# Performance work log

Hardware: AMD Instinct MI355X
Metric: run time of the kernel (lower is better)

The kernel has to match this reference:

```python
import jax, jax.numpy as jnp
import numpy as np

D_MODEL = 1024
NUM_HEADS = 16
D_K = D_MODEL // NUM_HEADS


def setup_inputs() -> dict:
    key = jax.random.key(0)
    ks = jax.random.split(key, 5)
    B, S = 4, 2048
    scale = 1.0 / np.sqrt(D_MODEL)
    x = jax.random.normal(ks[0], (B, S, D_MODEL), dtype=jnp.float32)
    Wq = jax.random.normal(ks[1], (D_MODEL, D_MODEL), dtype=jnp.float32) * scale
    Wk = jax.random.normal(ks[2], (D_MODEL, D_MODEL), dtype=jnp.float32) * scale
    Wv = jax.random.normal(ks[3], (D_MODEL, D_MODEL), dtype=jnp.float32) * scale
    Wo = jax.random.normal(ks[4], (D_MODEL, D_MODEL), dtype=jnp.float32) * scale
    return {"x": x, "Wq": Wq, "Wk": Wk, "Wv": Wv, "Wo": Wo}


def reference(x, Wq, Wk, Wv, Wo):
    B, S, _ = x.shape
    # projections (torch Linear: y = x @ W^T, no bias)
    def proj(W):
        y = jnp.einsum('bsd,ed->bse', x, W)
        # split heads: (b, s, h*dk) -> (b, h, s, dk)
        return y.reshape(B, S, NUM_HEADS, D_K).transpose(0, 2, 1, 3)
    Q, K, V = proj(Wq), proj(Wk), proj(Wv)
    scores = jnp.einsum('bhqd,bhkd->bhqk', Q, K) / np.sqrt(D_K)
    causal = jnp.tril(jnp.ones((S, S), dtype=bool))
    scores = jnp.where(causal, scores, -jnp.inf)
    attn = jax.nn.softmax(scores, axis=-1)
    out = jnp.einsum('bhqk,bhkd->bhqd', attn, V)
    out = out.transpose(0, 2, 1, 3).reshape(B, S, D_MODEL)
    return jnp.einsum('bse,de->bsd', out, Wo)
```

## Files before the change

### kernel.cpp

```cpp
#include <hip/hip_runtime.h>
#include <hip/hip_bf16.h>

typedef __attribute__((ext_vector_type(8))) short short8;
typedef __attribute__((ext_vector_type(4))) float f32x4;
typedef __attribute__((ext_vector_type(16))) float f32x16;

static constexpr int DM = 1024;
static constexpr int NH = 16;
static constexpr int DK = 64;
static constexpr int SL = 2048;
static constexpr int BB = 4;
static constexpr size_t QKV_ELEMS = (size_t)BB * NH * SL * DK;
static constexpr float NEG_BIG = -30000.0f;
static constexpr float SC_LOG2E = 0.125f * 1.44269504088896340736f;

union PackB { __hip_bfloat16 h[8]; uint4 u; };
union Pack4 { __hip_bfloat16 h[4]; uint2 u; };

typedef __attribute__((address_space(1))) unsigned int gu32;
typedef __attribute__((address_space(3))) unsigned int lu32;
__device__ __forceinline__ void async_copy16(const void* g, void* l) {
    __builtin_amdgcn_global_load_lds((gu32*)g, (lu32*)l, 16, 0, 0);
}

__device__ __forceinline__ unsigned cvt_pk_bf16(float lo, float hi) {
    unsigned r;
    asm("v_cvt_pk_bf16_f32 %0, %1, %2" : "=v"(r) : "v"(lo), "v"(hi));
    return r;
}
__device__ __forceinline__ void pl32_swap(unsigned &a, unsigned &b) {
    asm("v_permlane32_swap_b32 %0, %1" : "+v"(a), "+v"(b));
}

__global__ __launch_bounds__(256)
void cvt_all(const float* __restrict__ x,
             const float* __restrict__ wq, const float* __restrict__ wk,
             const float* __restrict__ wv, const float* __restrict__ wo,
             __hip_bfloat16* __restrict__ dst)
{
    const size_t i = (size_t)blockIdx.x * 256 + threadIdx.x;
    const float* src; size_t local;
    if (i < 2097152) { src = x; local = i; }
    else {
        const size_t j = i - 2097152;
        const int r = (int)(j >> 18);
        local = j & 262143;
        src = (r == 0) ? wq : (r == 1) ? wk : (r == 2) ? wv : wo;
    }
    float4 f = reinterpret_cast<const float4*>(src)[local];
    Pack4 p;
    p.h[0] = __float2bfloat16(f.x); p.h[1] = __float2bfloat16(f.y);
    p.h[2] = __float2bfloat16(f.z); p.h[3] = __float2bfloat16(f.w);
    reinterpret_cast<uint2*>(dst)[i] = p.u;
}

__global__ __launch_bounds__(256)
void gemm_qkv(const __hip_bfloat16* __restrict__ A,
              const __hip_bfloat16* __restrict__ W,
              __hip_bfloat16* __restrict__ q_out,
              __hip_bfloat16* __restrict__ k_out,
              __hip_bfloat16* __restrict__ v_out)
{
    __shared__ __hip_bfloat16 As[128 * 64];
    __shared__ __hip_bfloat16 Bs[128 * 64];
    const int tid  = threadIdx.x;
    const int m0   = blockIdx.x * 128;
    const int n0   = blockIdx.y * 128;
    const int w    = tid >> 6;
    const int lane = tid & 63;
    const int quad = lane >> 4;
    const int ln   = lane & 15;
    const int wm   = (w & 1) * 64;
    const int wn   = (w >> 1) * 64;
    const int srow = lane >> 3;
    const int sch  = ((lane & 7) ^ srow) * 8;

    f32x4 acc[4][4] = {};

    for (int k0 = 0; k0 < DM; k0 += 64) {
        #pragma unroll
        for (int j = 0; j < 4; j++) {
            const int rbase = w * 32 + j * 8;
            async_copy16(A + (size_t)(m0 + rbase + srow) * DM + k0 + sch,
                         &As[rbase * 64]);
            async_copy16(W + (size_t)(n0 + rbase + srow) * DM + k0 + sch,
                         &Bs[rbase * 64]);
        }
        __syncthreads();

        #pragma unroll
        for (int ks = 0; ks < 2; ks++) {
            short8 a[4], b[4];
            #pragma unroll
            for (int i = 0; i < 4; i++)
                a[i] = *reinterpret_cast<const short8*>(
                    &As[(wm + i*16 + ln) * 64 + (((ks*4 + quad) ^ (ln & 7)) * 8)]);
            #pragma unroll
            for (int j = 0; j < 4; j++)
                b[j] = *reinterpret_cast<const short8*>(
                    &Bs[(wn + j*16 + ln) * 64 + (((ks*4 + quad) ^ (ln & 7)) * 8)]);
            #pragma unroll
            for (int i = 0; i < 4; i++)
                #pragma unroll
                for (int j = 0; j < 4; j++)
                    acc[i][j] = __builtin_amdgcn_mfma_f32_16x16x32_bf16(a[i], b[j], acc[i][j], 0, 0, 0);
        }
        __syncthreads();
    }

    #pragma unroll
    for (int i = 0; i < 4; i++) {
        #pragma unroll
        for (int j = 0; j < 4; j++) {
            #pragma unroll
            for (int r = 0; r < 4; r++) {
                const int m = m0 + wm + i*16 + quad*4 + r;
                const int n = n0 + wn + j*16 + ln;
                const int b_ = m >> 11;
                const int s  = m & 2047;
                const int which = n >> 10;
                const int nn = n & 1023;
                const int h  = nn >> 6;
                const int d  = nn & 63;
                const __hip_bfloat16 v = __float2bfloat16(acc[i][j][r]);
                if (which == 0)
                    q_out[((size_t)((b_*NH + h)*SL + s))*DK + d] = v;
                else if (which == 1)
                    k_out[((size_t)((b_*NH + h)*SL + s))*DK + d] = v;
                else
                    v_out[((size_t)((b_*NH + h)*DK + d))*SL + s] = v;
            }
        }
    }
}

__global__ __launch_bounds__(256)
void gemm_wo(const __hip_bfloat16* __restrict__ A,
             const __hip_bfloat16* __restrict__ W,
             float* __restrict__ outp)
{
    __shared__ __hip_bfloat16 As[128 * 64];
    __shared__ __hip_bfloat16 Bs[128 * 64];
    const int tid  = threadIdx.x;
    const int m0   = blockIdx.x * 128;
    const int n0   = blockIdx.y * 128;
    const int w    = tid >> 6;
    const int lane = tid & 63;
    const int quad = lane >> 4;
    const int ln   = lane & 15;
    const int wm   = (w & 1) * 64;
    const int wn   = (w >> 1) * 64;
    const int srow = lane >> 3;
    const int sch  = ((lane & 7) ^ srow) * 8;

    f32x4 acc[4][4] = {};

    for (int k0 = 0; k0 < DM; k0 += 64) {
        #pragma unroll
        for (int j = 0; j < 4; j++) {
            const int rbase = w * 32 + j * 8;
            async_copy16(A + (size_t)(m0 + rbase + srow) * DM + k0 + sch,
                         &As[rbase * 64]);
            async_copy16(W + (size_t)(n0 + rbase + srow) * DM + k0 + sch,
                         &Bs[rbase * 64]);
        }
        __syncthreads();

        #pragma unroll
        for (int ks = 0; ks < 2; ks++) {
            short8 a[4], b[4];
            #pragma unroll
            for (int i = 0; i < 4; i++)
                a[i] = *reinterpret_cast<const short8*>(
                    &As[(wm + i*16 + ln) * 64 + (((ks*4 + quad) ^ (ln & 7)) * 8)]);
            #pragma unroll
            for (int j = 0; j < 4; j++)
                b[j] = *reinterpret_cast<const short8*>(
                    &Bs[(wn + j*16 + ln) * 64 + (((ks*4 + quad) ^ (ln & 7)) * 8)]);
            #pragma unroll
            for (int i = 0; i < 4; i++)
                #pragma unroll
                for (int j = 0; j < 4; j++)
                    acc[i][j] = __builtin_amdgcn_mfma_f32_16x16x32_bf16(a[i], b[j], acc[i][j], 0, 0, 0);
        }
        __syncthreads();
    }

    #pragma unroll
    for (int i = 0; i < 4; i++)
        #pragma unroll
        for (int j = 0; j < 4; j++)
            #pragma unroll
            for (int r = 0; r < 4; r++) {
                const int m = m0 + wm + i*16 + quad*4 + r;
                const int n = n0 + wn + j*16 + ln;
                outp[(size_t)m * DM + n] = acc[i][j][r];
            }
}

template<bool A_BF16, int MODE>
__global__ __launch_bounds__(256)
void gemm_bt(const void* __restrict__ Ap,
             const float* __restrict__ W,
             void* __restrict__ outp)
{
    __shared__ __hip_bfloat16 As[128][40];
    __shared__ __hip_bfloat16 Bs[128][40];
    const int tid  = threadIdx.x;
    const int m0   = blockIdx.x * 128;
    const int n0   = blockIdx.y * 128;
    const int w    = tid >> 6;
    const int lane = tid & 63;
    const int quad = lane >> 4;
    const int ln   = lane & 15;
    const int wm   = (w & 1) * 64;
    const int wn   = (w >> 1) * 64;
    const int lr   = tid >> 1;
    const int lc   = (tid & 1) * 16;

    f32x4 acc[4][4] = {};

    for (int k0 = 0; k0 < DM; k0 += 32) {
        if (A_BF16) {
            const uint4* ap = reinterpret_cast<const uint4*>(
                (const __hip_bfloat16*)Ap + (size_t)(m0 + lr) * DM + k0 + lc);
            uint4 a0 = ap[0], a1 = ap[1];
            *reinterpret_cast<uint4*>(&As[lr][lc])     = a0;
            *reinterpret_cast<uint4*>(&As[lr][lc + 8]) = a1;
        } else {
            const float4* ap = reinterpret_cast<const float4*>(
                (const float*)Ap + (size_t)(m0 + lr) * DM + k0 + lc);
            float4 f0 = ap[0], f1 = ap[1], f2 = ap[2], f3 = ap[3];
            PackB p0, p1;
            p0.h[0] = __float2bfloat16(f0.x); p0.h[1] = __float2bfloat16(f0.y);
            p0.h[2] = __float2bfloat16(f0.z); p0.h[3] = __float2bfloat16(f0.w);
            p0.h[4] = __float2bfloat16(f1.x); p0.h[5] = __float2bfloat16(f1.y);
            p0.h[6] = __float2bfloat16(f1.z); p0.h[7] = __float2bfloat16(f1.w);
            p1.h[0] = __float2bfloat16(f2.x); p1.h[1] = __float2bfloat16(f2.y);
            p1.h[2] = __float2bfloat16(f2.z); p1.h[3] = __float2bfloat16(f2.w);
            p1.h[4] = __float2bfloat16(f3.x); p1.h[5] = __float2bfloat16(f3.y);
            p1.h[6] = __float2bfloat16(f3.z); p1.h[7] = __float2bfloat16(f3.w);
            *reinterpret_cast<uint4*>(&As[lr][lc])     = p0.u;
            *reinterpret_cast<uint4*>(&As[lr][lc + 8]) = p1.u;
        }
        {
            const float4* wp = reinterpret_cast<const float4*>(
                W + (size_t)(n0 + lr) * DM + k0 + lc);
            float4 f0 = wp[0], f1 = wp[1], f2 = wp[2], f3 = wp[3];
            PackB p0, p1;
            p0.h[0] = __float2bfloat16(f0.x); p0.h[1] = __float2bfloat16(f0.y);
            p0.h[2] = __float2bfloat16(f0.z); p0.h[3] = __float2bfloat16(f0.w);
            p0.h[4] = __float2bfloat16(f1.x); p0.h[5] = __float2bfloat16(f1.y);
            p0.h[6] = __float2bfloat16(f1.z); p0.h[7] = __float2bfloat16(f1.w);
            p1.h[0] = __float2bfloat16(f2.x); p1.h[1] = __float2bfloat16(f2.y);
            p1.h[2] = __float2bfloat16(f2.z); p1.h[3] = __float2bfloat16(f2.w);
            p1.h[4] = __float2bfloat16(f3.x); p1.h[5] = __float2bfloat16(f3.y);
            p1.h[6] = __float2bfloat16(f3.z); p1.h[7] = __float2bfloat16(f3.w);
            *reinterpret_cast<uint4*>(&Bs[lr][lc])     = p0.u;
            *reinterpret_cast<uint4*>(&Bs[lr][lc + 8]) = p1.u;
        }
        __syncthreads();

        short8 a[4], b[4];
        #pragma unroll
        for (int i = 0; i < 4; i++)
            a[i] = *reinterpret_cast<const short8*>(&As[wm + i*16 + ln][quad*8]);
        #pragma unroll
        for (int j = 0; j < 4; j++)
            b[j] = *reinterpret_cast<const short8*>(&Bs[wn + j*16 + ln][quad*8]);
        #pragma unroll
        for (int i = 0; i < 4; i++)
            #pragma unroll
            for (int j = 0; j < 4; j++)
                acc[i][j] = __builtin_amdgcn_mfma_f32_16x16x32_bf16(a[i], b[j], acc[i][j], 0, 0, 0);
        __syncthreads();
    }

    #pragma unroll
    for (int i = 0; i < 4; i++) {
        #pragma unroll
        for (int j = 0; j < 4; j++) {
            #pragma unroll
            for (int r = 0; r < 4; r++) {
                const int m = m0 + wm + i*16 + quad*4 + r;
                const int n = n0 + wn + j*16 + ln;
                const float v = acc[i][j][r];
                if (MODE == 2) {
                    ((float*)outp)[(size_t)m * DM + n] = v;
                } else {
                    const int b_ = m >> 11;
                    const int s  = m & 2047;
                    const int h  = n >> 6;
                    const int d  = n & 63;
                    size_t idx;
                    if (MODE == 0) idx = ((size_t)((b_*NH + h)*SL + s))*DK + d;
                    else           idx = ((size_t)((b_*NH + h)*DK + d))*SL + s;
                    ((__hip_bfloat16*)outp)[idx] = __float2bfloat16(v);
                }
            }
        }
    }
}

__global__ __launch_bounds__(256)
void attn_causal(const __hip_bfloat16* __restrict__ Q,
                 const __hip_bfloat16* __restrict__ K,
                 const __hip_bfloat16* __restrict__ Vt,
                 __hip_bfloat16* __restrict__ O)
{
    __shared__ __hip_bfloat16 Ks[64][72];
    __shared__ __hip_bfloat16 Vs[64][72];

    const int tid  = threadIdx.x;
    const int w    = tid >> 6;
    const int lane = tid & 63;
    const int ln32 = lane & 31;
    const int hi   = lane >> 5;
    const int bh   = blockIdx.y;
    const int b_   = bh >> 4;
    const int h    = bh & 15;

    const int sr = tid >> 3;
    const int sc = (tid & 7) * 8;

    const __hip_bfloat16* Qb = Q  + (size_t)bh * SL * DK;
    const __hip_bfloat16* Kb = K  + (size_t)bh * SL * DK;
    const __hip_bfloat16* Vb = Vt + (size_t)bh * DK * SL;

    for (int pass = 0; pass < 2; ++pass) {
        const int qt    = (pass == 0) ? (int)blockIdx.x : 15 - (int)blockIdx.x;
        const int q0    = qt * 128;
        const int qbase = q0 + w * 32;
        const int qg    = qbase + ln32;

        short8 qf[4];
        #pragma unroll
        for (int dt = 0; dt < 4; dt++)
            qf[dt] = *reinterpret_cast<const short8*>(
                Qb + (size_t)qg * DK + dt*16 + hi*8);

        f32x16 o0 = {}, o1 = {};
        float lsum = 0.f;

        const int nkt = 2*qt + 2;

        uint4 kr0 = *reinterpret_cast<const uint4*>(Kb + (size_t)sr * DK + sc);
        uint4 kr1 = *reinterpret_cast<const uint4*>(Kb + (size_t)(32 + sr) * DK + sc);
        uint4 vr0 = *reinterpret_cast<const uint4*>(Vb + (size_t)sr * SL + sc);
        uint4 vr1 = *reinterpret_cast<const uint4*>(Vb + (size_t)(32 + sr) * SL + sc);

        for (int it = 0; it < nkt; ++it) {
            const int k0 = it * 64;
            __syncthreads();
            *reinterpret_cast<uint4*>(&Ks[sr     ][sc]) = kr0;
            *reinterpret_cast<uint4*>(&Ks[sr + 32][sc]) = kr1;
            *reinterpret_cast<uint4*>(&Vs[sr     ][sc]) = vr0;
            *reinterpret_cast<uint4*>(&Vs[sr + 32][sc]) = vr1;
            __syncthreads();
            if (it + 1 < nkt) {
                const int kn = k0 + 64;
                kr0 = *reinterpret_cast<const uint4*>(Kb + (size_t)(kn + sr) * DK + sc);
                kr1 = *reinterpret_cast<const uint4*>(Kb + (size_t)(kn + 32 + sr) * DK + sc);
                vr0 = *reinterpret_cast<const uint4*>(Vb + (size_t)sr * SL + kn + sc);
                vr1 = *reinterpret_cast<const uint4*>(Vb + (size_t)(32 + sr) * SL + kn + sc);
            }
            if (k0 > qbase + 31) continue;

            f32x16 s0 = {}, s1 = {};
            __builtin_amdgcn_s_setprio(1);
            #pragma unroll
            for (int dt = 0; dt < 4; dt++) {
                short8 kf0 = *reinterpret_cast<const short8*>(&Ks[ln32     ][dt*16 + hi*8]);
                short8 kf1 = *reinterpret_cast<const short8*>(&Ks[32 + ln32][dt*16 + hi*8]);
                s0 = __builtin_amdgcn_mfma_f32_32x32x16_bf16(kf0, qf[dt], s0, 0, 0, 0);
                s1 = __builtin_amdgcn_mfma_f32_32x32x16_bf16(kf1, qf[dt], s1, 0, 0, 0);
            }
            __builtin_amdgcn_s_setprio(0);

            const bool dodiag = (k0 + 63 > qbase);
            if (dodiag) {
                #pragma unroll
                for (int r = 0; r < 16; r++) {
                    const int km = (r & 3) + 8*(r >> 2) + 4*hi;
                    float v0 = s0[r] * SC_LOG2E;
                    float v1 = s1[r] * SC_LOG2E;
                    if (k0 + km      > qg) v0 = NEG_BIG;
                    if (k0 + 32 + km > qg) v1 = NEG_BIG;
                    const float p0 = __builtin_amdgcn_exp2f(v0);
                    const float p1 = __builtin_amdgcn_exp2f(v1);
                    s0[r] = p0; s1[r] = p1;
                    lsum += p0 + p1;
                }
            } else {
                #pragma unroll
                for (int r = 0; r < 16; r++) {
                    const float p0 = __builtin_amdgcn_exp2f(s0[r] * SC_LOG2E);
                    const float p1 = __builtin_amdgcn_exp2f(s1[r] * SC_LOG2E);
                    s0[r] = p0; s1[r] = p1;
                    lsum += p0 + p1;
                }
            }

            __builtin_amdgcn_s_setprio(1);
            #pragma unroll
            for (int c = 0; c < 4; c++) {
                const int R = 8 * (c & 1);
                unsigned x0, x1, y0, y1;
                if (c < 2) {
                    x0 = cvt_pk_bf16(s0[R+0], s0[R+1]);
                    x1 = cvt_pk_bf16(s0[R+2], s0[R+3]);
                    y0 = cvt_pk_bf16(s0[R+4], s0[R+5]);
                    y1 = cvt_pk_bf16(s0[R+6], s0[R+7]);
                } else {
                    x0 = cvt_pk_bf16(s1[R+0], s1[R+1]);
                    x1 = cvt_pk_bf16(s1[R+2], s1[R+3]);
                    y0 = cvt_pk_bf16(s1[R+4], s1[R+5]);
                    y1 = cvt_pk_bf16(s1[R+6], s1[R+7]);
                }
                pl32_swap(x0, y0);
                pl32_swap(x1, y1);
                union { unsigned u[4]; short8 s8; } pf;
                pf.u[0] = x0; pf.u[1] = x1; pf.u[2] = y0; pf.u[3] = y1;
                short8 vf0 = *reinterpret_cast<const short8*>(&Vs[ln32     ][c*16 + hi*8]);
                short8 vf1 = *reinterpret_cast<const short8*>(&Vs[32 + ln32][c*16 + hi*8]);
                o0 = __builtin_amdgcn_mfma_f32_32x32x16_bf16(vf0, pf.s8, o0, 0, 0, 0);
                o1 = __builtin_amdgcn_mfma_f32_32x32x16_bf16(vf1, pf.s8, o1, 0, 0, 0);
            }
            __builtin_amdgcn_s_setprio(0);
        }

        const float ls = lsum + __shfl_xor(lsum, 32, 64);
        const float rq = 1.0f / ls;

        __hip_bfloat16* Orow = O + (((size_t)b_ * SL + qg) * NH + h) * DK;
        #pragma unroll
        for (int g = 0; g < 4; g++) {
            uint2 pk0, pk1;
            pk0.x = cvt_pk_bf16(o0[4*g+0]*rq, o0[4*g+1]*rq);
            pk0.y = cvt_pk_bf16(o0[4*g+2]*rq, o0[4*g+3]*rq);
            pk1.x = cvt_pk_bf16(o1[4*g+0]*rq, o1[4*g+1]*rq);
            pk1.y = cvt_pk_bf16(o1[4*g+2]*rq, o1[4*g+3]*rq);
            *reinterpret_cast<uint2*>(Orow + 8*g + 4*hi)      = pk0;
            *reinterpret_cast<uint2*>(Orow + 32 + 8*g + 4*hi) = pk1;
        }
    }
}

extern "C" void kernel_launch(void* const* d_in, const int* in_sizes, int n_in,
                              void* d_out, int out_size, void* d_ws, size_t ws_size,
                              hipStream_t stream)
{
    const float* x  = (const float*)d_in[0];
    const float* Wq = (const float*)d_in[1];
    const float* Wk = (const float*)d_in[2];
    const float* Wv = (const float*)d_in[3];
    const float* Wo = (const float*)d_in[4];

    __hip_bfloat16* q_ws = (__hip_bfloat16*)d_ws;
    __hip_bfloat16* k_ws = q_ws + QKV_ELEMS;
    __hip_bfloat16* v_ws = k_ws + QKV_ELEMS;

    const dim3 gb(256);
    const size_t FAST_WS = (3 * QKV_ELEMS + QKV_ELEMS + 4 * (size_t)DM * DM)
                           * sizeof(__hip_bfloat16);

    if (ws_size >= FAST_WS) {
        __hip_bfloat16* xb  = v_ws + QKV_ELEMS;
        __hip_bfloat16* wqb = xb  + QKV_ELEMS;
        __hip_bfloat16* wob = wqb + 3 * (size_t)DM * DM;

        cvt_all<<<12288, 256, 0, stream>>>(x, Wq, Wk, Wv, Wo, xb);

        gemm_qkv<<<dim3(64, 24), gb, 0, stream>>>(xb, wqb, q_ws, k_ws, v_ws);

        attn_causal<<<dim3(8, BB*NH), 256, 0, stream>>>(q_ws, k_ws, v_ws, xb);

        gemm_wo<<<dim3(64, 8), gb, 0, stream>>>(xb, wob, (float*)d_out);
    } else {
        __hip_bfloat16* obuf = (__hip_bfloat16*)d_out;
        float*          fbuf = (float*)d_ws;
        const dim3 gg(64, 8);
        gemm_bt<false, 0><<<gg, gb, 0, stream>>>(x, Wq, q_ws);
        gemm_bt<false, 0><<<gg, gb, 0, stream>>>(x, Wk, k_ws);
        gemm_bt<false, 1><<<gg, gb, 0, stream>>>(x, Wv, v_ws);
        attn_causal<<<dim3(8, BB*NH), 256, 0, stream>>>(q_ws, k_ws, v_ws, obuf);
        gemm_bt<true, 2><<<gg, gb, 0, stream>>>(obuf, Wo, fbuf);
        (void)hipMemcpyAsync(d_out, fbuf, QKV_ELEMS * sizeof(float),
                             hipMemcpyDeviceToDevice, stream);
    }
}
```

Measured before the change: 256.3 us.

## Double-buffer LDS and enlarge GEMM tiles to 256x128 with 512 threads

Both bf16 GEMMs (QKV projection and output projection) now use 512-thread blocks computing 256x128 tiles. Shared-memory staging is double-buffered, so the async global-to-LDS load for the next K slice overlaps the MFMAs on the current one. The per-slice pair of __syncthreads is replaced by one vmcnt wait plus barrier. MFMA sections are wrapped in s_setprio to favour the math waves. This costs twice the LDS per block (96 KB) and halves the grid, which may limit occupancy and leave the wave count uneven across CUs.

```diff
diff --git a/kernel.cpp b/kernel.cpp
--- a/kernel.cpp
+++ b/kernel.cpp
@@ -54,39 +54,52 @@
     reinterpret_cast<uint2*>(dst)[i] = p.u;
 }
 
-__global__ __launch_bounds__(256)
+__global__ __launch_bounds__(512, 2)
 void gemm_qkv(const __hip_bfloat16* __restrict__ A,
               const __hip_bfloat16* __restrict__ W,
               __hip_bfloat16* __restrict__ q_out,
               __hip_bfloat16* __restrict__ k_out,
               __hip_bfloat16* __restrict__ v_out)
 {
-    __shared__ __hip_bfloat16 As[128 * 64];
-    __shared__ __hip_bfloat16 Bs[128 * 64];
+    __shared__ __hip_bfloat16 As[2][256 * 64];
+    __shared__ __hip_bfloat16 Bs[2][128 * 64];
     const int tid  = threadIdx.x;
-    const int m0   = blockIdx.x * 128;
+    const int m0   = blockIdx.x * 256;
     const int n0   = blockIdx.y * 128;
     const int w    = tid >> 6;
     const int lane = tid & 63;
     const int quad = lane >> 4;
     const int ln   = lane & 15;
-    const int wm   = (w & 1) * 64;
-    const int wn   = (w >> 1) * 64;
+    const int wm   = (w & 3) * 64;
+    const int wn   = (w >> 2) * 64;
     const int srow = lane >> 3;
     const int sch  = ((lane & 7) ^ srow) * 8;
 
     f32x4 acc[4][4] = {};
 
-    for (int k0 = 0; k0 < DM; k0 += 64) {
+    auto stage = [&](int buf, int k0) {
         #pragma unroll
         for (int j = 0; j < 4; j++) {
             const int rbase = w * 32 + j * 8;
             async_copy16(A + (size_t)(m0 + rbase + srow) * DM + k0 + sch,
-                         &As[rbase * 64]);
+                         &As[buf][rbase * 64]);
+        }
+        #pragma unroll
+        for (int j = 0; j < 2; j++) {
+            const int rbase = w * 16 + j * 8;
             async_copy16(W + (size_t)(n0 + rbase + srow) * DM + k0 + sch,
-                         &Bs[rbase * 64]);
-        }
-        __syncthreads();
+                         &Bs[buf][rbase * 64]);
+        }
+    };
+
+    constexpr int NT = DM / 64;
+    stage(0, 0);
+    asm volatile("s_waitcnt vmcnt(0)" ::: "memory");
+    __builtin_amdgcn_s_barrier();
+
+    int cur = 0;
+    for (int t = 0; t < NT; ++t) {
+        if (t + 1 < NT) stage(cur ^ 1, (t + 1) * 64);
 
         #pragma unroll
         for (int ks = 0; ks < 2; ks++) {
@@ -94,18 +107,25 @@
             #pragma unroll
             for (int i = 0; i < 4; i++)
                 a[i] = *reinterpret_cast<const short8*>(
-                    &As[(wm + i*16 + ln) * 64 + (((ks*4 + quad) ^ (ln & 7)) * 8)]);
+                    &As[cur][(wm + i*16 + ln) * 64 + (((ks*4 + quad) ^ (ln & 7)) * 8)]);
             #pragma unroll
             for (int j = 0; j < 4; j++)
                 b[j] = *reinterpret_cast<const short8*>(
-                    &Bs[(wn + j*16 + ln) * 64 + (((ks*4 + quad) ^ (ln & 7)) * 8)]);
+                    &Bs[cur][(wn + j*16 + ln) * 64 + (((ks*4 + quad) ^ (ln & 7)) * 8)]);
+            __builtin_amdgcn_s_setprio(1);
             #pragma unroll
             for (int i = 0; i < 4; i++)
                 #pragma unroll
                 for (int j = 0; j < 4; j++)
                     acc[i][j] = __builtin_amdgcn_mfma_f32_16x16x32_bf16(a[i], b[j], acc[i][j], 0, 0, 0);
-        }
-        __syncthreads();
+            __builtin_amdgcn_s_setprio(0);
+        }
+
+        if (t + 1 < NT) {
+            asm volatile("s_waitcnt vmcnt(0)" ::: "memory");
+            __builtin_amdgcn_s_barrier();
+        }
+        cur ^= 1;
     }
 
     #pragma unroll
@@ -134,37 +154,50 @@
     }
 }
 
-__global__ __launch_bounds__(256)
+__global__ __launch_bounds__(512, 2)
 void gemm_wo(const __hip_bfloat16* __restrict__ A,
              const __hip_bfloat16* __restrict__ W,
              float* __restrict__ outp)
 {
-    __shared__ __hip_bfloat16 As[128 * 64];
-    __shared__ __hip_bfloat16 Bs[128 * 64];
+    __shared__ __hip_bfloat16 As[2][256 * 64];
+    __shared__ __hip_bfloat16 Bs[2][128 * 64];
     const int tid  = threadIdx.x;
-    const int m0   = blockIdx.x * 128;
+    const int m0   = blockIdx.x * 256;
     const int n0   = blockIdx.y * 128;
     const int w    = tid >> 6;
     const int lane = tid & 63;
     const int quad = lane >> 4;
     const int ln   = lane & 15;
-    const int wm   = (w & 1) * 64;
-    const int wn   = (w >> 1) * 64;
+    const int wm   = (w & 3) * 64;
+    const int wn   = (w >> 2) * 64;
     const int srow = lane >> 3;
     const int sch  = ((lane & 7) ^ srow) * 8;
 
     f32x4 acc[4][4] = {};
 
-    for (int k0 = 0; k0 < DM; k0 += 64) {
+    auto stage = [&](int buf, int k0) {
         #pragma unroll
         for (int j = 0; j < 4; j++) {
             const int rbase = w * 32 + j * 8;
             async_copy16(A + (size_t)(m0 + rbase + srow) * DM + k0 + sch,
-                         &As[rbase * 64]);
+                         &As[buf][rbase * 64]);
+        }
+        #pragma unroll
+        for (int j = 0; j < 2; j++) {
+            const int rbase = w * 16 + j * 8;
             async_copy16(W + (size_t)(n0 + rbase + srow) * DM + k0 + sch,
-                         &Bs[rbase * 64]);
-        }
-        __syncthreads();
+                         &Bs[buf][rbase * 64]);
+        }
+    };
+
+    constexpr int NT = DM / 64;
+    stage(0, 0);
+    asm volatile("s_waitcnt vmcnt(0)" ::: "memory");
+    __builtin_amdgcn_s_barrier();
+
+    int cur = 0;
+    for (int t = 0; t < NT; ++t) {
+        if (t + 1 < NT) stage(cur ^ 1, (t + 1) * 64);
 
         #pragma unroll
         for (int ks = 0; ks < 2; ks++) {
@@ -172,18 +205,25 @@
             #pragma unroll
             for (int i = 0; i < 4; i++)
                 a[i] = *reinterpret_cast<const short8*>(
-                    &As[(wm + i*16 + ln) * 64 + (((ks*4 + quad) ^ (ln & 7)) * 8)]);
+                    &As[cur][(wm + i*16 + ln) * 64 + (((ks*4 + quad) ^ (ln & 7)) * 8)]);
             #pragma unroll
             for (int j = 0; j < 4; j++)
                 b[j] = *reinterpret_cast<const short8*>(
-                    &Bs[(wn + j*16 + ln) * 64 + (((ks*4 + quad) ^ (ln & 7)) * 8)]);
+                    &Bs[cur][(wn + j*16 + ln) * 64 + (((ks*4 + quad) ^ (ln & 7)) * 8)]);
+            __builtin_amdgcn_s_setprio(1);
             #pragma unroll
             for (int i = 0; i < 4; i++)
                 #pragma unroll
                 for (int j = 0; j < 4; j++)
                     acc[i][j] = __builtin_amdgcn_mfma_f32_16x16x32_bf16(a[i], b[j], acc[i][j], 0, 0, 0);
-        }
-        __syncthreads();
+            __builtin_amdgcn_s_setprio(0);
+        }
+
+        if (t + 1 < NT) {
+            asm volatile("s_waitcnt vmcnt(0)" ::: "memory");
+            __builtin_amdgcn_s_barrier();
+        }
+        cur ^= 1;
     }
 
     #pragma unroll
@@ -460,7 +500,6 @@
     __hip_bfloat16* k_ws = q_ws + QKV_ELEMS;
     __hip_bfloat16* v_ws = k_ws + QKV_ELEMS;
 
-    const dim3 gb(256);
     const size_t FAST_WS = (3 * QKV_ELEMS + QKV_ELEMS + 4 * (size_t)DM * DM)
                            * sizeof(__hip_bfloat16);
 
@@ -471,15 +510,16 @@
 
         cvt_all<<<12288, 256, 0, stream>>>(x, Wq, Wk, Wv, Wo, xb);
 
-        gemm_qkv<<<dim3(64, 24), gb, 0, stream>>>(xb, wqb, q_ws, k_ws, v_ws);
+        gemm_qkv<<<dim3(32, 24), dim3(512), 0, stream>>>(xb, wqb, q_ws, k_ws, v_ws);
 
         attn_causal<<<dim3(8, BB*NH), 256, 0, stream>>>(q_ws, k_ws, v_ws, xb);
 
-        gemm_wo<<<dim3(64, 8), gb, 0, stream>>>(xb, wob, (float*)d_out);
+        gemm_wo<<<dim3(32, 8), dim3(512), 0, stream>>>(xb, wob, (float*)d_out);
     } else {
         __hip_bfloat16* obuf = (__hip_bfloat16*)d_out;
         float*          fbuf = (float*)d_ws;
         const dim3 gg(64, 8);
+        const dim3 gb(256);
         gemm_bt<false, 0><<<gg, gb, 0, stream>>>(x, Wq, q_ws);
         gemm_bt<false, 0><<<gg, gb, 0, stream>>>(x, Wk, k_ws);
         gemm_bt<false, 1><<<gg, gb, 0, stream>>>(x, Wv, v_ws);
```

Result: slower. 262.2 us (+2.3%).

## Fold softmax scale into Q projection and process 128-key tiles per sync

Applied to the files above, without the earlier changes.

The softmax scale times log2(e) is now applied to Q in the projection epilogue, so the attention kernel no longer multiplies every score before exp2. The attention loop loads 128 keys (two 64-key halves) per stage, which halves the number of barrier pairs and LDS refill rounds. The row sum is split into two accumulators to shorten the add dependency chain. In exchange the kernel uses more LDS and more prefetch registers, which may lower occupancy, and Q is rounded to bf16 after scaling, which slightly changes numerics.

```diff
diff --git a/kernel.cpp b/kernel.cpp
--- a/kernel.cpp
+++ b/kernel.cpp
@@ -2,6 +2,7 @@
 #include <hip/hip_bf16.h>
 
 typedef __attribute__((ext_vector_type(8))) short short8;
+typedef __attribute__((ext_vector_type(2))) float f32x2;
 typedef __attribute__((ext_vector_type(4))) float f32x4;
 typedef __attribute__((ext_vector_type(16))) float f32x16;
 
@@ -122,13 +123,16 @@
                 const int nn = n & 1023;
                 const int h  = nn >> 6;
                 const int d  = nn & 63;
-                const __hip_bfloat16 v = __float2bfloat16(acc[i][j][r]);
-                if (which == 0)
+                if (which == 0) {
+                    const __hip_bfloat16 v = __float2bfloat16(acc[i][j][r] * SC_LOG2E);
                     q_out[((size_t)((b_*NH + h)*SL + s))*DK + d] = v;
-                else if (which == 1)
+                } else if (which == 1) {
+                    const __hip_bfloat16 v = __float2bfloat16(acc[i][j][r]);
                     k_out[((size_t)((b_*NH + h)*SL + s))*DK + d] = v;
-                else
+                } else {
+                    const __hip_bfloat16 v = __float2bfloat16(acc[i][j][r]);
                     v_out[((size_t)((b_*NH + h)*DK + d))*SL + s] = v;
+                }
             }
         }
     }
@@ -202,7 +206,7 @@
 __global__ __launch_bounds__(256)
 void gemm_bt(const void* __restrict__ Ap,
              const float* __restrict__ W,
-             void* __restrict__ outp)
+             void* __restrict__ outp, float scl)
 {
     __shared__ __hip_bfloat16 As[128][40];
     __shared__ __hip_bfloat16 Bs[128][40];
@@ -284,7 +288,7 @@
             for (int r = 0; r < 4; r++) {
                 const int m = m0 + wm + i*16 + quad*4 + r;
                 const int n = n0 + wn + j*16 + ln;
-                const float v = acc[i][j][r];
+                const float v = acc[i][j][r] * scl;
                 if (MODE == 2) {
                     ((float*)outp)[(size_t)m * DM + n] = v;
                 } else {
@@ -308,8 +312,8 @@
                  const __hip_bfloat16* __restrict__ Vt,
                  __hip_bfloat16* __restrict__ O)
 {
-    __shared__ __hip_bfloat16 Ks[64][72];
-    __shared__ __hip_bfloat16 Vs[64][72];
+    __shared__ __hip_bfloat16 Ks[128][72];
+    __shared__ __hip_bfloat16 Vs[64][136];
 
     const int tid  = threadIdx.x;
     const int w    = tid >> 6;
@@ -340,95 +344,113 @@
                 Qb + (size_t)qg * DK + dt*16 + hi*8);
 
         f32x16 o0 = {}, o1 = {};
-        float lsum = 0.f;
-
-        const int nkt = 2*qt + 2;
-
-        uint4 kr0 = *reinterpret_cast<const uint4*>(Kb + (size_t)sr * DK + sc);
-        uint4 kr1 = *reinterpret_cast<const uint4*>(Kb + (size_t)(32 + sr) * DK + sc);
-        uint4 vr0 = *reinterpret_cast<const uint4*>(Vb + (size_t)sr * SL + sc);
-        uint4 vr1 = *reinterpret_cast<const uint4*>(Vb + (size_t)(32 + sr) * SL + sc);
-
-        for (int it = 0; it < nkt; ++it) {
-            const int k0 = it * 64;
+        f32x2 ls2 = {0.f, 0.f};
+
+        const int npair = qt + 1;
+
+        uint4 ka = *reinterpret_cast<const uint4*>(Kb + (size_t)(sr     ) * DK + sc);
+        uint4 kb = *reinterpret_cast<const uint4*>(Kb + (size_t)(sr + 32) * DK + sc);
+        uint4 kc = *reinterpret_cast<const uint4*>(Kb + (size_t)(sr + 64) * DK + sc);
+        uint4 kd = *reinterpret_cast<const uint4*>(Kb + (size_t)(sr + 96) * DK + sc);
+        uint4 va = *reinterpret_cast<const uint4*>(Vb + (size_t)(sr     ) * SL + sc);
+        uint4 vb = *reinterpret_cast<const uint4*>(Vb + (size_t)(sr + 32) * SL + sc);
+        uint4 vc = *reinterpret_cast<const uint4*>(Vb + (size_t)(sr     ) * SL + 64 + sc);
+        uint4 vd = *reinterpret_cast<const uint4*>(Vb + (size_t)(sr + 32) * SL + 64 + sc);
+
+        for (int ip = 0; ip < npair; ++ip) {
+            const int k0 = ip * 128;
             __syncthreads();
-            *reinterpret_cast<uint4*>(&Ks[sr     ][sc]) = kr0;
-            *reinterpret_cast<uint4*>(&Ks[sr + 32][sc]) = kr1;
-            *reinterpret_cast<uint4*>(&Vs[sr     ][sc]) = vr0;
-            *reinterpret_cast<uint4*>(&Vs[sr + 32][sc]) = vr1;
+            *reinterpret_cast<uint4*>(&Ks[sr      ][sc]) = ka;
+            *reinterpret_cast<uint4*>(&Ks[sr +  32][sc]) = kb;
+            *reinterpret_cast<uint4*>(&Ks[sr +  64][sc]) = kc;
+            *reinterpret_cast<uint4*>(&Ks[sr +  96][sc]) = kd;
+            *reinterpret_cast<uint4*>(&Vs[sr      ][sc]) = va;
+            *reinterpret_cast<uint4*>(&Vs[sr +  32][sc]) = vb;
+            *reinterpret_cast<uint4*>(&Vs[sr      ][64 + sc]) = vc;
+            *reinterpret_cast<uint4*>(&Vs[sr +  32][64 + sc]) = vd;
             __syncthreads();
-            if (it + 1 < nkt) {
-                const int kn = k0 + 64;
-                kr0 = *reinterpret_cast<const uint4*>(Kb + (size_t)(kn + sr) * DK + sc);
-                kr1 = *reinterpret_cast<const uint4*>(Kb + (size_t)(kn + 32 + sr) * DK + sc);
-                vr0 = *reinterpret_cast<const uint4*>(Vb + (size_t)sr * SL + kn + sc);
-                vr1 = *reinterpret_cast<const uint4*>(Vb + (size_t)(32 + sr) * SL + kn + sc);
+            if (ip + 1 < npair) {
+                const int kn = k0 + 128;
+                ka = *reinterpret_cast<const uint4*>(Kb + (size_t)(kn + sr     ) * DK + sc);
+                kb = *reinterpret_cast<const uint4*>(Kb + (size_t)(kn + sr + 32) * DK + sc);
+                kc = *reinterpret_cast<const uint4*>(Kb + (size_t)(kn + sr + 64) * DK + sc);
+                kd = *reinterpret_cast<const uint4*>(Kb + (size_t)(kn + sr + 96) * DK + sc);
+                va = *reinterpret_cast<const uint4*>(Vb + (size_t)(sr     ) * SL + kn + sc);
+                vb = *reinterpret_cast<const uint4*>(Vb + (size_t)(sr + 32) * SL + kn + sc);
+                vc = *reinterpret_cast<const uint4*>(Vb + (size_t)(sr     ) * SL + kn + 64 + sc);
+                vd = *reinterpret_cast<const uint4*>(Vb + (size_t)(sr + 32) * SL + kn + 64 + sc);
             }
-            if (k0 > qbase + 31) continue;
-
-            f32x16 s0 = {}, s1 = {};
-            __builtin_amdgcn_s_setprio(1);
-            #pragma unroll
-            for (int dt = 0; dt < 4; dt++) {
-                short8 kf0 = *reinterpret_cast<const short8*>(&Ks[ln32     ][dt*16 + hi*8]);
-                short8 kf1 = *reinterpret_cast<const short8*>(&Ks[32 + ln32][dt*16 + hi*8]);
-                s0 = __builtin_amdgcn_mfma_f32_32x32x16_bf16(kf0, qf[dt], s0, 0, 0, 0);
-                s1 = __builtin_amdgcn_mfma_f32_32x32x16_bf16(kf1, qf[dt], s1, 0, 0, 0);
+
+            #pragma unroll
+            for (int hf = 0; hf < 2; hf++) {
+                const int kh0 = k0 + hf * 64;
+                if (kh0 > qbase + 31) continue;
+
+                f32x16 s0 = {}, s1 = {};
+                __builtin_amdgcn_s_setprio(1);
+                #pragma unroll
+                for (int dt = 0; dt < 4; dt++) {
+                    short8 kf0 = *reinterpret_cast<const short8*>(&Ks[hf*64 +      ln32][dt*16 + hi*8]);
+                    short8 kf1 = *reinterpret_cast<const short8*>(&Ks[hf*64 + 32 + ln32][dt*16 + hi*8]);
+                    s0 = __builtin_amdgcn_mfma_f32_32x32x16_bf16(kf0, qf[dt], s0, 0, 0, 0);
+                    s1 = __builtin_amdgcn_mfma_f32_32x32x16_bf16(kf1, qf[dt], s1, 0, 0, 0);
+                }
+                __builtin_amdgcn_s_setprio(0);
+
+                const bool dodiag = (kh0 + 63 > qbase);
+                if (dodiag) {
+                    #pragma unroll
+                    for (int r = 0; r < 16; r++) {
+                        const int km = (r & 3) + 8*(r >> 2) + 4*hi;
+                        float v0 = s0[r];
+                        float v1 = s1[r];
+                        if (kh0 + km      > qg) v0 = NEG_BIG;
+                        if (kh0 + 32 + km > qg) v1 = NEG_BIG;
+                        const float p0 = __builtin_amdgcn_exp2f(v0);
+                        const float p1 = __builtin_amdgcn_exp2f(v1);
+                        s0[r] = p0; s1[r] = p1;
+                        ls2.x += p0; ls2.y += p1;
+                    }
+                } else {
+                    #pragma unroll
+                    for (int r = 0; r < 16; r++) {
+                        const float p0 = __builtin_amdgcn_exp2f(s0[r]);
+                        const float p1 = __builtin_amdgcn_exp2f(s1[r]);
+                        s0[r] = p0; s1[r] = p1;
+                        ls2.x += p0; ls2.y += p1;
+                    }
+                }
+
+                __builtin_amdgcn_s_setprio(1);
+                #pragma unroll
+                for (int c = 0; c < 4; c++) {
+                    const int R = 8 * (c & 1);
+                    unsigned x0, x1, y0, y1;
+                    if (c < 2) {
+                        x0 = cvt_pk_bf16(s0[R+0], s0[R+1]);
+                        x1 = cvt_pk_bf16(s0[R+2], s0[R+3]);
+                        y0 = cvt_pk_bf16(s0[R+4], s0[R+5]);
+                        y1 = cvt_pk_bf16(s0[R+6], s0[R+7]);
+                    } else {
+                        x0 = cvt_pk_bf16(s1[R+0], s1[R+1]);
+                        x1 = cvt_pk_bf16(s1[R+2], s1[R+3]);
+                        y0 = cvt_pk_bf16(s1[R+4], s1[R+5]);
+                        y1 = cvt_pk_bf16(s1[R+6], s1[R+7]);
+                    }
+                    pl32_swap(x0, y0);
+                    pl32_swap(x1, y1);
+                    union { unsigned u[4]; short8 s8; } pf;
+                    pf.u[0] = x0; pf.u[1] = x1; pf.u[2] = y0; pf.u[3] = y1;
+                    short8 vf0 = *reinterpret_cast<const short8*>(&Vs[ln32     ][hf*64 + c*16 + hi*8]);
+                    short8 vf1 = *reinterpret_cast<const short8*>(&Vs[32 + ln32][hf*64 + c*16 + hi*8]);
+                    o0 = __builtin_amdgcn_mfma_f32_32x32x16_bf16(vf0, pf.s8, o0, 0, 0, 0);
+                    o1 = __builtin_amdgcn_mfma_f32_32x32x16_bf16(vf1, pf.s8, o1, 0, 0, 0);
+                }
+                __builtin_amdgcn_s_setprio(0);
             }
-            __builtin_amdgcn_s_setprio(0);
-
-            const bool dodiag = (k0 + 63 > qbase);
-            if (dodiag) {
-                #pragma unroll
-                for (int r = 0; r < 16; r++) {
-                    const int km = (r & 3) + 8*(r >> 2) + 4*hi;
-                    float v0 = s0[r] * SC_LOG2E;
-                    float v1 = s1[r] * SC_LOG2E;
-                    if (k0 + km      > qg) v0 = NEG_BIG;
-                    if (k0 + 32 + km > qg) v1 = NEG_BIG;
-                    const float p0 = __builtin_amdgcn_exp2f(v0);
-                    const float p1 = __builtin_amdgcn_exp2f(v1);
-                    s0[r] = p0; s1[r] = p1;
-                    lsum += p0 + p1;
-                }
-            } else {
-                #pragma unroll
-                for (int r = 0; r < 16; r++) {
-                    const float p0 = __builtin_amdgcn_exp2f(s0[r] * SC_LOG2E);
-                    const float p1 = __builtin_amdgcn_exp2f(s1[r] * SC_LOG2E);
-                    s0[r] = p0; s1[r] = p1;
-                    lsum += p0 + p1;
-                }
-            }
-
-            __builtin_amdgcn_s_setprio(1);
-            #pragma unroll
-            for (int c = 0; c < 4; c++) {
-                const int R = 8 * (c & 1);
-                unsigned x0, x1, y0, y1;
-                if (c < 2) {
-                    x0 = cvt_pk_bf16(s0[R+0], s0[R+1]);
-                    x1 = cvt_pk_bf16(s0[R+2], s0[R+3]);
-                    y0 = cvt_pk_bf16(s0[R+4], s0[R+5]);
-                    y1 = cvt_pk_bf16(s0[R+6], s0[R+7]);
-                } else {
-                    x0 = cvt_pk_bf16(s1[R+0], s1[R+1]);
-                    x1 = cvt_pk_bf16(s1[R+2], s1[R+3]);
-                    y0 = cvt_pk_bf16(s1[R+4], s1[R+5]);
-                    y1 = cvt_pk_bf16(s1[R+6], s1[R+7]);
-                }
-                pl32_swap(x0, y0);
-                pl32_swap(x1, y1);
-                union { unsigned u[4]; short8 s8; } pf;
-                pf.u[0] = x0; pf.u[1] = x1; pf.u[2] = y0; pf.u[3] = y1;
-                short8 vf0 = *reinterpret_cast<const short8*>(&Vs[ln32     ][c*16 + hi*8]);
-                short8 vf1 = *reinterpret_cast<const short8*>(&Vs[32 + ln32][c*16 + hi*8]);
-                o0 = __builtin_amdgcn_mfma_f32_32x32x16_bf16(vf0, pf.s8, o0, 0, 0, 0);
-                o1 = __builtin_amdgcn_mfma_f32_32x32x16_bf16(vf1, pf.s8, o1, 0, 0, 0);
-            }
-            __builtin_amdgcn_s_setprio(0);
-        }
-
+        }
+
+        float lsum = ls2.x + ls2.y;
         const float ls = lsum + __shfl_xor(lsum, 32, 64);
         const float rq = 1.0f / ls;
 
@@ -480,11 +502,11 @@
         __hip_bfloat16* obuf = (__hip_bfloat16*)d_out;
         float*          fbuf = (float*)d_ws;
         const dim3 gg(64, 8);
-        gemm_bt<false, 0><<<gg, gb, 0, stream>>>(x, Wq, q_ws);
-        gemm_bt<false, 0><<<gg, gb, 0, stream>>>(x, Wk, k_ws);
-        gemm_bt<false, 1><<<gg, gb, 0, stream>>>(x, Wv, v_ws);
+        gemm_bt<false, 0><<<gg, gb, 0, stream>>>(x, Wq, q_ws, SC_LOG2E);
+        gemm_bt<false, 0><<<gg, gb, 0, stream>>>(x, Wk, k_ws, 1.0f);
+        gemm_bt<false, 1><<<gg, gb, 0, stream>>>(x, Wv, v_ws, 1.0f);
         attn_causal<<<dim3(8, BB*NH), 256, 0, stream>>>(q_ws, k_ws, v_ws, obuf);
-        gemm_bt<true, 2><<<gg, gb, 0, stream>>>(obuf, Wo, fbuf);
+        gemm_bt<true, 2><<<gg, gb, 0, stream>>>(obuf, Wo, fbuf, 1.0f);
         (void)hipMemcpyAsync(d_out, fbuf, QKV_ELEMS * sizeof(float),
                              hipMemcpyDeviceToDevice, stream);
     }
```

New measurement: 255.7 us. No clear change (-0.2%).
